# Kernel optimization log

Measured on AMD Instinct MI355X. Metric: run time of the kernel, lower is better.

## Reference

```python
import jax, jax.numpy as jnp
import numpy as np
import math

B, S, H, D = 4, 4096, 1024, 128

def setup_inputs() -> dict:
    key = jax.random.key(0)
    ks = jax.random.split(key, 4)
    scale = 1.0 / math.sqrt(H)
    return {
        "x": jax.random.normal(ks[0], (B, S, H), dtype=jnp.float32),
        "Wk": jax.random.normal(ks[1], (H, D), dtype=jnp.float32) * scale,
        "bk": jnp.zeros((D,), dtype=jnp.float32),
        "Wq": jax.random.normal(ks[2], (H, D), dtype=jnp.float32) * scale,
        "bq": jnp.zeros((D,), dtype=jnp.float32),
        "Wv": jax.random.normal(ks[3], (H, D), dtype=jnp.float32) * scale,
        "bv": jnp.zeros((D,), dtype=jnp.float32),
    }

def reference(x, Wk, bk, Wq, bq, Wv, bv):
    seq_len = x.shape[1]
    k = x @ Wk + bk                     # [B,S,D]
    q = x @ Wq + bq                     # [B,S,D]
    v = x @ Wv + bv                     # [B,S,D]
    scores = jnp.einsum('bqd,bkd->bqk', q, k) / jnp.sqrt(jnp.float32(q.shape[-1]))
    causal = jnp.tril(jnp.ones((seq_len, seq_len), dtype=bool))
    scores = jnp.where(causal, scores, -jnp.inf)
    attn = jax.nn.softmax(scores, axis=-1)  # dropout p=0.0 -> identity
    return jnp.einsum('bqk,bkd->bqd', attn, v)
```

## Files before the change

### kernel.cpp

```cpp
#include <hip/hip_runtime.h>
#include <hip/hip_bf16.h>

typedef __attribute__((ext_vector_type(8))) __bf16 bf16x8;
typedef __attribute__((ext_vector_type(4))) float f32x4;

#define QSCALE (0.08838834764831845f * 1.4426950408889634f)
#define SLOT_BYTES 33792

static __device__ __forceinline__ int pack2(float a, float b) {
    union { __bf16 h[2]; int u; } x;
    x.h[0] = (__bf16)a; x.h[1] = (__bf16)b;
    return x.u;
}

static __device__ __forceinline__ void softmax_strip(f32x4 (&s)[4], float& mr, float& lr,
                                                     f32x4 (&o)[8], int hi) {
    float mloc = s[0][0];
#pragma unroll
    for (int ct = 0; ct < 4; ++ct)
#pragma unroll
        for (int r = 0; r < 4; ++r) mloc = fmaxf(mloc, s[ct][r]);
    mloc = fmaxf(mloc, __shfl_xor(mloc, 16));
    mloc = fmaxf(mloc, __shfl_xor(mloc, 32));

    float alpha = 1.f;
    if (!__all(mloc <= mr + 8.f)) {
        const float mn = fmaxf(mr, mloc);
        alpha = exp2f(mr - mn);
        mr = mn;
        float ao[4];
#pragma unroll
        for (int r = 0; r < 4; ++r) ao[r] = __shfl(alpha, hi * 4 + r);
#pragma unroll
        for (int dt = 0; dt < 8; ++dt)
#pragma unroll
            for (int r = 0; r < 4; ++r) o[dt][r] *= ao[r];
    }
    float rs = 0.f;
#pragma unroll
    for (int ct = 0; ct < 4; ++ct)
#pragma unroll
        for (int r = 0; r < 4; ++r) {
            const float pv = exp2f(s[ct][r] - mr);
            s[ct][r] = pv;
            rs += pv;
        }
    rs += __shfl_xor(rs, 16);
    rs += __shfl_xor(rs, 32);
    lr = lr * alpha + rs;
}

static __device__ __forceinline__ void store_v_perm(__bf16* V_lds, int row, int u, bf16x8 val) {
    union { bf16x8 v; int2 d[2]; } x; x.v = val;
    const int ua  = 4 * (u >> 2) + 2 * (u & 1);
    const int off = ((u >> 1) & 1) * 8;
    const int sw  = row & 7;
    char* base = (char*)V_lds + row * 128;
    *reinterpret_cast<int2*>(base + ((ua ^ sw) << 4) + off)       = x.d[0];
    *reinterpret_cast<int2*>(base + (((ua + 1) ^ sw) << 4) + off) = x.d[1];
}

__global__ __launch_bounds__(256) void prep_w(const float* __restrict__ Wq,
                                              const float* __restrict__ Wk,
                                              const float* __restrict__ Wv,
                                              __bf16* __restrict__ Wt) {
    __shared__ float tile[32][33];
    const int bid = blockIdx.x;
    const int p   = bid >> 7;
    const int rem = bid & 127;
    const int kt  = rem >> 2;
    const int ct  = rem & 3;
    const float* W = (p == 0) ? Wq : ((p == 1) ? Wk : Wv);
    const int tr = threadIdx.x >> 5;
    const int tc = threadIdx.x & 31;
#pragma unroll
    for (int pass = 0; pass < 4; ++pass) {
        const int k = kt * 32 + pass * 8 + tr;
        tile[pass * 8 + tr][tc] = W[k * 128 + ct * 32 + tc];
    }
    __syncthreads();
#pragma unroll
    for (int pass = 0; pass < 4; ++pass) {
        const int c = ct * 32 + pass * 8 + tr;
        Wt[p * 131072 + c * 1024 + kt * 32 + tc] = (__bf16)tile[tc][pass * 8 + tr];
    }
}

__global__ __launch_bounds__(512, 4) void qkv_gemm(const float* __restrict__ x,
                                                   const __bf16* __restrict__ Wt,
                                                   const float* __restrict__ bq,
                                                   const float* __restrict__ bk,
                                                   const float* __restrict__ bv,
                                                   __bf16* __restrict__ qws,
                                                   __bf16* __restrict__ kws,
                                                   __bf16* __restrict__ vT) {
    __shared__ __align__(16) char smem[53248];
    __bf16* B_lds = (__bf16*)smem;
    __bf16* A_lds = (__bf16*)(smem + 49152);

    const int tid = threadIdx.x;
    const int w   = tid >> 6;
    const int l   = tid & 63;
    const int lo  = l & 15;
    const int hi  = l >> 4;
    const int r0  = blockIdx.x * 32;
    const int wr  = w >> 2;
    const int wc  = w & 3;

    const int arow = tid >> 4, aq = tid & 15;

    bf16x8 bst[6];
    float4 ast;

    auto STAGE_LOAD = [&](int ks) {
#pragma unroll
        for (int j = 0; j < 6; ++j) {
            const int n = w * 6 + j;
            const int c = n * 8 + (l >> 3);
            const int u = l & 7;
            bst[j] = *reinterpret_cast<const bf16x8*>(
                Wt + (size_t)c * 1024 + ks * 64 + u * 8);
        }
        ast = *reinterpret_cast<const float4*>(
            x + (size_t)(r0 + arow) * 1024 + ks * 64 + aq * 4);
    };
    auto STAGE_WRITE = [&]() {
#pragma unroll
        for (int j = 0; j < 6; ++j) {
            const int n = w * 6 + j;
            const int c = n * 8 + (l >> 3);
            const int u = l & 7;
            *reinterpret_cast<bf16x8*>(&B_lds[c * 64 + ((u ^ (c & 7)) << 3)]) = bst[j];
        }
        union { __bf16 h[4]; int2 d; } av;
        av.h[0] = (__bf16)ast.x; av.h[1] = (__bf16)ast.y;
        av.h[2] = (__bf16)ast.z; av.h[3] = (__bf16)ast.w;
        *reinterpret_cast<int2*>((char*)A_lds + arow * 128 +
            (((aq >> 1) ^ (arow & 7)) << 4) + ((aq & 1) << 3)) = av.d;
    };

    f32x4 acc[6];
#pragma unroll
    for (int tt = 0; tt < 6; ++tt) acc[tt] = (f32x4){0.f, 0.f, 0.f, 0.f};

    STAGE_LOAD(0);
    STAGE_WRITE();
    __syncthreads();

    const int lr = wr * 16 + lo;
    for (int ks = 0; ks < 16; ++ks) {
        if (ks < 15) STAGE_LOAD(ks + 1);

#pragma unroll
        for (int kc = 0; kc < 2; ++kc) {
            bf16x8 a = *reinterpret_cast<const bf16x8*>(
                &A_lds[lr * 64 + (((kc * 4 + hi) ^ (lr & 7)) << 3)]);
#pragma unroll
            for (int tt = 0; tt < 6; ++tt) {
                const int c = (wc * 6 + tt) * 16 + lo;
                bf16x8 b = *reinterpret_cast<const bf16x8*>(
                    &B_lds[c * 64 + (((kc * 4 + hi) ^ (c & 7)) << 3)]);
                acc[tt] = __builtin_amdgcn_mfma_f32_16x16x32_bf16(a, b, acc[tt], 0, 0, 0);
            }
        }
        __syncthreads();
        if (ks < 15) {
            STAGE_WRITE();
            __syncthreads();
        }
    }

    __bf16* ob = (__bf16*)smem;
#pragma unroll
    for (int tt = 0; tt < 6; ++tt) {
        const int t    = wc * 6 + tt;
        const int proj = t >> 3;
        const int col  = (t & 7) * 16 + lo;
        const float* bias = (proj == 0) ? bq : ((proj == 1) ? bk : bv);
        const float bb = bias[col];
        const float sc = (proj == 0) ? QSCALE : 1.f;
#pragma unroll
        for (int r = 0; r < 4; ++r) {
            const int row = wr * 16 + hi * 4 + r;
            ob[row * 392 + t * 16 + lo] = (__bf16)((acc[tt][r] + bb) * sc);
        }
    }
    __syncthreads();

    {
        const int row = tid >> 4;
        const int ch  = tid & 15;
        bf16x8 vq = *reinterpret_cast<const bf16x8*>(&ob[row * 392 + ch * 8]);
        bf16x8 vk = *reinterpret_cast<const bf16x8*>(&ob[row * 392 + 128 + ch * 8]);
        *reinterpret_cast<bf16x8*>(&qws[(size_t)(r0 + row) * 128 + ch * 8]) = vq;
        *reinterpret_cast<bf16x8*>(&kws[(size_t)(r0 + row) * 128 + ch * 8]) = vk;
    }
    {
        const int col = tid >> 2;
        const int rc  = tid & 3;
        bf16x8 vv;
#pragma unroll
        for (int j = 0; j < 8; ++j)
            vv[j] = ob[(rc * 8 + j) * 392 + 256 + col];
        const int b_ = r0 >> 12;
        const int s0 = r0 & 4095;
        *reinterpret_cast<bf16x8*>(
            &vT[(size_t)b_ * 524288 + (size_t)col * 4096 + s0 + rc * 8]) = vv;
    }
}

__global__ __launch_bounds__(512, 4) void attn(const __bf16* __restrict__ qws,
                                               const __bf16* __restrict__ kws,
                                               const __bf16* __restrict__ vT,
                                               char* __restrict__ part,
                                               float* __restrict__ out,
                                               int NSEG, int SEG, int direct) {
    __shared__ __align__(16) __bf16 K_lds[2][64 * 128];
    __shared__ __align__(16) __bf16 V_lds[2][128 * 64];

    const int tid = threadIdx.x;
    const int w   = tid >> 6;
    const int l   = tid & 63;
    const int lo  = l & 15;
    const int hi  = l >> 4;

    const int sidx = blockIdx.x / NSEG;
    const int seg  = blockIdx.x - sidx * NSEG;
    const int batch = sidx & 3;
    const int mblk  = 31 - (sidx >> 2);
    const int q0    = mblk * 128;
    const int extent = q0 + 128;

    const int kv_start = seg * SEG;
    if (kv_start >= extent) return;
    const int kv_end = min(kv_start + SEG, extent);
    const int t0 = kv_start >> 6;
    const int t1 = (kv_end + 63) >> 6;

    const int rw = q0 + w * 16;

    const int tKrow = tid >> 3;
    const int tKu   = (tid & 7) * 2;
    const int tVrow = tid >> 2;
    const int tVu   = (tid & 3) * 2;

    const __bf16* kb = kws + (size_t)batch * 524288;
    const __bf16* vb = vT  + (size_t)batch * 524288;

    const size_t qoff = (size_t)(batch * 4096 + rw + lo) * 128 + hi * 8;
    bf16x8 qf[4];
#pragma unroll
    for (int dc = 0; dc < 4; ++dc)
        qf[dc] = *reinterpret_cast<const bf16x8*>(qws + qoff + dc * 32);

    {
        const int kvb = t0 * 64;
        bf16x8 k0 = *reinterpret_cast<const bf16x8*>(kb + (size_t)(kvb + tKrow) * 128 + tKu * 8);
        bf16x8 k1 = *reinterpret_cast<const bf16x8*>(kb + (size_t)(kvb + tKrow) * 128 + tKu * 8 + 8);
        bf16x8 v0 = *reinterpret_cast<const bf16x8*>(vb + (size_t)tVrow * 4096 + kvb + tVu * 8);
        bf16x8 v1 = *reinterpret_cast<const bf16x8*>(vb + (size_t)tVrow * 4096 + kvb + tVu * 8 + 8);
        *reinterpret_cast<bf16x8*>(&K_lds[0][tKrow * 128 + ((tKu       ^ (tKrow & 7)) * 8)]) = k0;
        *reinterpret_cast<bf16x8*>(&K_lds[0][tKrow * 128 + (((tKu + 1) ^ (tKrow & 7)) * 8)]) = k1;
        store_v_perm(V_lds[0], tVrow, tVu,     v0);
        store_v_perm(V_lds[0], tVrow, tVu + 1, v1);
        __syncthreads();
    }

    f32x4 o[8];
#pragma unroll
    for (int dt = 0; dt < 8; ++dt) o[dt] = (f32x4){0.f, 0.f, 0.f, 0.f};
    float mr = -__builtin_inff();
    float lr = 0.f;

    int cur = 0;
    for (int t = t0; t < t1; ++t) {
        const int kvb = t * 64;
        const bool pfetch = (t + 1 < t1);

        bf16x8 kr0, kr1, vr0, vr1;
        if (pfetch) {
            const int kvn = kvb + 64;
            kr0 = *reinterpret_cast<const bf16x8*>(kb + (size_t)(kvn + tKrow) * 128 + tKu * 8);
            kr1 = *reinterpret_cast<const bf16x8*>(kb + (size_t)(kvn + tKrow) * 128 + tKu * 8 + 8);
            vr0 = *reinterpret_cast<const bf16x8*>(vb + (size_t)tVrow * 4096 + kvn + tVu * 8);
            vr1 = *reinterpret_cast<const bf16x8*>(vb + (size_t)tVrow * 4096 + kvn + tVu * 8 + 8);
        }

        if (kvb <= rw + 15) {
            f32x4 s[4];
#pragma unroll
            for (int ct = 0; ct < 4; ++ct) s[ct] = (f32x4){0.f, 0.f, 0.f, 0.f};
            const int sw = lo & 7;
            __builtin_amdgcn_s_setprio(1);
#pragma unroll
            for (int ct = 0; ct < 4; ++ct) {
                const int rbase = (ct * 16 + lo) * 128;
#pragma unroll
                for (int dc = 0; dc < 4; ++dc) {
                    bf16x8 kf = *reinterpret_cast<const bf16x8*>(
                        &K_lds[cur][rbase + (((dc * 4 + hi) ^ sw) << 3)]);
                    s[ct] = __builtin_amdgcn_mfma_f32_16x16x32_bf16(kf, qf[dc], s[ct], 0, 0, 0);
                }
            }
            __builtin_amdgcn_s_setprio(0);

            if (kvb + 63 > rw) {
#pragma unroll
                for (int ct = 0; ct < 4; ++ct)
#pragma unroll
                    for (int r = 0; r < 4; ++r)
                        if (kvb + ct * 16 + hi * 4 + r > rw + lo)
                            s[ct][r] = -__builtin_inff();
            }

            softmax_strip(s, mr, lr, o, hi);

            union { int u[4]; bf16x8 v; } pf0, pf1;
            pf0.u[0] = pack2(s[0][0], s[0][1]);
            pf0.u[1] = pack2(s[0][2], s[0][3]);
            pf0.u[2] = pack2(s[1][0], s[1][1]);
            pf0.u[3] = pack2(s[1][2], s[1][3]);
            pf1.u[0] = pack2(s[2][0], s[2][1]);
            pf1.u[1] = pack2(s[2][2], s[2][3]);
            pf1.u[2] = pack2(s[3][0], s[3][1]);
            pf1.u[3] = pack2(s[3][2], s[3][3]);

            __builtin_amdgcn_s_setprio(1);
#pragma unroll
            for (int dt = 0; dt < 8; ++dt) {
                const int vbase = (dt * 16 + lo) * 64;
                bf16x8 vf0 = *reinterpret_cast<const bf16x8*>(
                    &V_lds[cur][vbase + ((hi ^ sw) << 3)]);
                o[dt] = __builtin_amdgcn_mfma_f32_16x16x32_bf16(pf0.v, vf0, o[dt], 0, 0, 0);
                bf16x8 vf1 = *reinterpret_cast<const bf16x8*>(
                    &V_lds[cur][vbase + (((4 + hi) ^ sw) << 3)]);
                o[dt] = __builtin_amdgcn_mfma_f32_16x16x32_bf16(pf1.v, vf1, o[dt], 0, 0, 0);
            }
            __builtin_amdgcn_s_setprio(0);
        }

        if (pfetch) {
            const int nxt = cur ^ 1;
            *reinterpret_cast<bf16x8*>(&K_lds[nxt][tKrow * 128 + ((tKu       ^ (tKrow & 7)) * 8)]) = kr0;
            *reinterpret_cast<bf16x8*>(&K_lds[nxt][tKrow * 128 + (((tKu + 1) ^ (tKrow & 7)) * 8)]) = kr1;
            store_v_perm(V_lds[nxt], tVrow, tVu,     vr0);
            store_v_perm(V_lds[nxt], tVrow, tVu + 1, vr1);
            __syncthreads();
            cur = nxt;
        }
    }

    float lro[4], mro[4];
#pragma unroll
    for (int r = 0; r < 4; ++r) {
        lro[r] = __shfl(lr, hi * 4 + r);
        mro[r] = __shfl(mr, hi * 4 + r);
    }

    if (direct) {
#pragma unroll
        for (int dt = 0; dt < 8; ++dt)
#pragma unroll
            for (int r = 0; r < 4; ++r) {
                const size_t row = (size_t)(batch * 4096 + rw + hi * 4 + r);
                out[row * 128 + dt * 16 + lo] = o[dt][r] / lro[r];
            }
    } else {
        char* slot = part + ((size_t)(sidx * NSEG + seg)) * SLOT_BYTES;
        __bf16* so = (__bf16*)slot;
        float*  sf = (float*)(slot + 32768);
        const int rb = w * 16 + hi * 4;
#pragma unroll
        for (int dt = 0; dt < 8; ++dt)
#pragma unroll
            for (int r = 0; r < 4; ++r)
                so[(rb + r) * 128 + dt * 16 + lo] = (__bf16)o[dt][r];
        if (lo == 0) {
#pragma unroll
            for (int r = 0; r < 4; ++r) {
                sf[rb + r]       = mro[r];
                sf[128 + rb + r] = lro[r];
            }
        }
    }
}

__global__ __launch_bounds__(256) void combine(const char* __restrict__ part,
                                               float* __restrict__ out,
                                               int NSEG, int SEG) {
    const int sidx = blockIdx.x >> 3;
    const int rg   = blockIdx.x & 7;
    const int batch = sidx & 3;
    const int mblk  = 31 - (sidx >> 2);
    const int extent = mblk * 128 + 128;
    const int nseg  = min(NSEG, (extent + SEG - 1) / SEG);

    const int rl = rg * 16 + (threadIdx.x >> 4);
    const int c0 = (threadIdx.x & 15) * 8;
    const char* base = part + (size_t)sidx * NSEG * SLOT_BYTES;

    float mj[8];
    float M = -__builtin_inff();
#pragma unroll 8
    for (int j = 0; j < 8; ++j) {
        if (j < nseg) {
            mj[j] = ((const float*)(base + j * SLOT_BYTES + 32768))[rl];
            M = fmaxf(M, mj[j]);
        }
    }
    float wj[8];
    float L = 0.f;
#pragma unroll 8
    for (int j = 0; j < 8; ++j) {
        if (j < nseg) {
            wj[j] = exp2f(mj[j] - M);
            L += ((const float*)(base + j * SLOT_BYTES + 32768))[128 + rl] * wj[j];
        }
    }

    float a[8];
#pragma unroll
    for (int e = 0; e < 8; ++e) a[e] = 0.f;
#pragma unroll 8
    for (int j = 0; j < 8; ++j) {
        if (j < nseg) {
            const bf16x8 ov = *reinterpret_cast<const bf16x8*>(
                base + j * SLOT_BYTES + (size_t)(rl * 128 + c0) * 2);
            const float wgt = wj[j];
#pragma unroll
            for (int e = 0; e < 8; ++e) a[e] += (float)ov[e] * wgt;
        }
    }
    const float inv = 1.f / L;
    float* op = out + ((size_t)(batch * 4096 + mblk * 128 + rl)) * 128 + c0;
    float4* o4 = reinterpret_cast<float4*>(op);
    o4[0] = (float4){a[0]*inv, a[1]*inv, a[2]*inv, a[3]*inv};
    o4[1] = (float4){a[4]*inv, a[5]*inv, a[6]*inv, a[7]*inv};
}

extern "C" void kernel_launch(void* const* d_in, const int* in_sizes, int n_in,
                              void* d_out, int out_size, void* d_ws, size_t ws_size,
                              hipStream_t stream) {
    const float* x  = (const float*)d_in[0];
    const float* Wk = (const float*)d_in[1];
    const float* bk = (const float*)d_in[2];
    const float* Wq = (const float*)d_in[3];
    const float* bq = (const float*)d_in[4];
    const float* Wv = (const float*)d_in[5];
    const float* bv = (const float*)d_in[6];
    float* out = (float*)d_out;

    char* ws = (char*)d_ws;
    __bf16* Wt  = (__bf16*)ws;
    __bf16* qws = (__bf16*)(ws + 786432);
    __bf16* kws = (__bf16*)(ws + 786432 + 4194304);
    __bf16* vT  = (__bf16*)(ws + 786432 + 2 * 4194304);
    const size_t base = 786432 + 3 * 4194304;

    const size_t per_seg = 128ull * SLOT_BYTES;
    int NSEG = 1;
    for (int cand = 8; cand >= 2; cand >>= 1) {
        if (base + (size_t)cand * per_seg <= ws_size) { NSEG = cand; break; }
    }
    char* part = ws + base;

    prep_w<<<384, 256, 0, stream>>>(Wq, Wk, Wv, Wt);
    qkv_gemm<<<512, 512, 0, stream>>>(x, Wt, bq, bk, bv, qws, kws, vT);

    if (NSEG >= 2) {
        const int SEG = 4096 / NSEG;
        attn<<<128 * NSEG, 512, 0, stream>>>(qws, kws, vT, part, out, NSEG, SEG, 0);
        combine<<<1024, 256, 0, stream>>>(part, out, NSEG, SEG);
    } else {
        attn<<<128, 512, 0, stream>>>(qws, kws, vT, nullptr, out, 1, 4096, 1);
    }
}
```

Before: 100.0 us.

## Double query rows per attention block and stage K via direct global-to-LDS loads

Each block now processes 256 query rows instead of 128, with every wave handling two 16-row strips that share the K and V fragments read from LDS. This halves K/V traffic per query row. K tiles are staged with global_load_lds directly into LDS, bypassing registers. The split-KV partitioning goes up to 16 segments, and the combine kernel and slot layout are resized to match. In exchange, accumulator register pressure roughly doubles, which can reduce occupancy. The second strip's Q is reloaded from global memory on every tile, and with fewer query blocks the causal load balance is coarser.

New measurement: 324.9 us. +224.8%, slower.

```diff
diff --git a/kernel.cpp b/kernel.cpp
--- a/kernel.cpp
+++ b/kernel.cpp
@@ -5,7 +5,7 @@
 typedef __attribute__((ext_vector_type(4))) float f32x4;
 
 #define QSCALE (0.08838834764831845f * 1.4426950408889634f)
-#define SLOT_BYTES 33792
+#define SLOT_BYTES 67584
 
 static __device__ __forceinline__ int pack2(float a, float b) {
     union { __bf16 h[2]; int u; } x;
@@ -227,9 +227,9 @@
     const int sidx = blockIdx.x / NSEG;
     const int seg  = blockIdx.x - sidx * NSEG;
     const int batch = sidx & 3;
-    const int mblk  = 31 - (sidx >> 2);
-    const int q0    = mblk * 128;
-    const int extent = q0 + 128;
+    const int mblk  = 15 - (sidx >> 2);
+    const int q0    = mblk * 256;
+    const int extent = q0 + 256;
 
     const int kv_start = seg * SEG;
     if (kv_start >= extent) return;
@@ -237,59 +237,84 @@
     const int t0 = kv_start >> 6;
     const int t1 = (kv_end + 63) >> 6;
 
-    const int rw = q0 + w * 16;
-
-    const int tKrow = tid >> 3;
-    const int tKu   = (tid & 7) * 2;
+    const int rwA = q0 + w * 32;
+    const int rwB = rwA + 16;
+
     const int tVrow = tid >> 2;
     const int tVu   = (tid & 3) * 2;
 
     const __bf16* kb = kws + (size_t)batch * 524288;
     const __bf16* vb = vT  + (size_t)batch * 524288;
 
-    const size_t qoff = (size_t)(batch * 4096 + rw + lo) * 128 + hi * 8;
-    bf16x8 qf[4];
+    auto stage_k = [&](int buf, int kvb) {
+#pragma unroll
+        for (int j = 0; j < 2; ++j) {
+            const int c   = w * 2 + j;
+            const int row = c * 4 + (l >> 4);
+            const int up  = l & 15;
+            const __bf16* g = kb + (size_t)(kvb + row) * 128 + ((up ^ (row & 7)) << 3);
+            __builtin_amdgcn_global_load_lds(
+                (const __attribute__((address_space(1))) void*)g,
+                (__attribute__((address_space(3))) void*)&K_lds[buf][c * 512],
+                16, 0, 0);
+        }
+    };
+
+    const size_t qoffA = (size_t)(batch * 4096 + rwA + lo) * 128 + hi * 8;
+    const size_t qoffB = qoffA + 16 * 128;
+    bf16x8 qfA[4];
 #pragma unroll
     for (int dc = 0; dc < 4; ++dc)
-        qf[dc] = *reinterpret_cast<const bf16x8*>(qws + qoff + dc * 32);
+        qfA[dc] = *reinterpret_cast<const bf16x8*>(qws + qoffA + dc * 32);
 
     {
         const int kvb = t0 * 64;
-        bf16x8 k0 = *reinterpret_cast<const bf16x8*>(kb + (size_t)(kvb + tKrow) * 128 + tKu * 8);
-        bf16x8 k1 = *reinterpret_cast<const bf16x8*>(kb + (size_t)(kvb + tKrow) * 128 + tKu * 8 + 8);
+        stage_k(0, kvb);
         bf16x8 v0 = *reinterpret_cast<const bf16x8*>(vb + (size_t)tVrow * 4096 + kvb + tVu * 8);
         bf16x8 v1 = *reinterpret_cast<const bf16x8*>(vb + (size_t)tVrow * 4096 + kvb + tVu * 8 + 8);
-        *reinterpret_cast<bf16x8*>(&K_lds[0][tKrow * 128 + ((tKu       ^ (tKrow & 7)) * 8)]) = k0;
-        *reinterpret_cast<bf16x8*>(&K_lds[0][tKrow * 128 + (((tKu + 1) ^ (tKrow & 7)) * 8)]) = k1;
         store_v_perm(V_lds[0], tVrow, tVu,     v0);
         store_v_perm(V_lds[0], tVrow, tVu + 1, v1);
         __syncthreads();
     }
 
-    f32x4 o[8];
-#pragma unroll
-    for (int dt = 0; dt < 8; ++dt) o[dt] = (f32x4){0.f, 0.f, 0.f, 0.f};
-    float mr = -__builtin_inff();
-    float lr = 0.f;
+    f32x4 oA[8], oB[8];
+#pragma unroll
+    for (int dt = 0; dt < 8; ++dt) {
+        oA[dt] = (f32x4){0.f, 0.f, 0.f, 0.f};
+        oB[dt] = (f32x4){0.f, 0.f, 0.f, 0.f};
+    }
+    float mrA = -__builtin_inff(), lrA = 0.f;
+    float mrB = -__builtin_inff(), lrB = 0.f;
 
     int cur = 0;
     for (int t = t0; t < t1; ++t) {
         const int kvb = t * 64;
         const bool pfetch = (t + 1 < t1);
-
-        bf16x8 kr0, kr1, vr0, vr1;
+        const int nxt = cur ^ 1;
+
+        bf16x8 vr0, vr1;
         if (pfetch) {
             const int kvn = kvb + 64;
-            kr0 = *reinterpret_cast<const bf16x8*>(kb + (size_t)(kvn + tKrow) * 128 + tKu * 8);
-            kr1 = *reinterpret_cast<const bf16x8*>(kb + (size_t)(kvn + tKrow) * 128 + tKu * 8 + 8);
+            stage_k(nxt, kvn);
             vr0 = *reinterpret_cast<const bf16x8*>(vb + (size_t)tVrow * 4096 + kvn + tVu * 8);
             vr1 = *reinterpret_cast<const bf16x8*>(vb + (size_t)tVrow * 4096 + kvn + tVu * 8 + 8);
         }
 
-        if (kvb <= rw + 15) {
-            f32x4 s[4];
-#pragma unroll
-            for (int ct = 0; ct < 4; ++ct) s[ct] = (f32x4){0.f, 0.f, 0.f, 0.f};
+        const bool doB = (kvb <= rwB + 15);
+        const bool doA = (kvb <= rwA + 15);
+
+        if (doB) {
+            bf16x8 qfB[4];
+#pragma unroll
+            for (int dc = 0; dc < 4; ++dc)
+                qfB[dc] = *reinterpret_cast<const bf16x8*>(qws + qoffB + dc * 32);
+
+            f32x4 sA[4], sB[4];
+#pragma unroll
+            for (int ct = 0; ct < 4; ++ct) {
+                sA[ct] = (f32x4){0.f, 0.f, 0.f, 0.f};
+                sB[ct] = (f32x4){0.f, 0.f, 0.f, 0.f};
+            }
             const int sw = lo & 7;
             __builtin_amdgcn_s_setprio(1);
 #pragma unroll
@@ -299,31 +324,51 @@
                 for (int dc = 0; dc < 4; ++dc) {
                     bf16x8 kf = *reinterpret_cast<const bf16x8*>(
                         &K_lds[cur][rbase + (((dc * 4 + hi) ^ sw) << 3)]);
-                    s[ct] = __builtin_amdgcn_mfma_f32_16x16x32_bf16(kf, qf[dc], s[ct], 0, 0, 0);
+                    sB[ct] = __builtin_amdgcn_mfma_f32_16x16x32_bf16(kf, qfB[dc], sB[ct], 0, 0, 0);
+                    if (doA)
+                        sA[ct] = __builtin_amdgcn_mfma_f32_16x16x32_bf16(kf, qfA[dc], sA[ct], 0, 0, 0);
                 }
             }
             __builtin_amdgcn_s_setprio(0);
 
-            if (kvb + 63 > rw) {
+            if (kvb + 63 > rwB) {
 #pragma unroll
                 for (int ct = 0; ct < 4; ++ct)
 #pragma unroll
                     for (int r = 0; r < 4; ++r)
-                        if (kvb + ct * 16 + hi * 4 + r > rw + lo)
-                            s[ct][r] = -__builtin_inff();
-            }
-
-            softmax_strip(s, mr, lr, o, hi);
-
-            union { int u[4]; bf16x8 v; } pf0, pf1;
-            pf0.u[0] = pack2(s[0][0], s[0][1]);
-            pf0.u[1] = pack2(s[0][2], s[0][3]);
-            pf0.u[2] = pack2(s[1][0], s[1][1]);
-            pf0.u[3] = pack2(s[1][2], s[1][3]);
-            pf1.u[0] = pack2(s[2][0], s[2][1]);
-            pf1.u[1] = pack2(s[2][2], s[2][3]);
-            pf1.u[2] = pack2(s[3][0], s[3][1]);
-            pf1.u[3] = pack2(s[3][2], s[3][3]);
+                        if (kvb + ct * 16 + hi * 4 + r > rwB + lo)
+                            sB[ct][r] = -__builtin_inff();
+            }
+            if (doA && kvb + 63 > rwA) {
+#pragma unroll
+                for (int ct = 0; ct < 4; ++ct)
+#pragma unroll
+                    for (int r = 0; r < 4; ++r)
+                        if (kvb + ct * 16 + hi * 4 + r > rwA + lo)
+                            sA[ct][r] = -__builtin_inff();
+            }
+
+            softmax_strip(sB, mrB, lrB, oB, hi);
+            union { int u[4]; bf16x8 v; } pfB0, pfB1, pfA0, pfA1;
+            pfB0.u[0] = pack2(sB[0][0], sB[0][1]);
+            pfB0.u[1] = pack2(sB[0][2], sB[0][3]);
+            pfB0.u[2] = pack2(sB[1][0], sB[1][1]);
+            pfB0.u[3] = pack2(sB[1][2], sB[1][3]);
+            pfB1.u[0] = pack2(sB[2][0], sB[2][1]);
+            pfB1.u[1] = pack2(sB[2][2], sB[2][3]);
+            pfB1.u[2] = pack2(sB[3][0], sB[3][1]);
+            pfB1.u[3] = pack2(sB[3][2], sB[3][3]);
+            if (doA) {
+                softmax_strip(sA, mrA, lrA, oA, hi);
+                pfA0.u[0] = pack2(sA[0][0], sA[0][1]);
+                pfA0.u[1] = pack2(sA[0][2], sA[0][3]);
+                pfA0.u[2] = pack2(sA[1][0], sA[1][1]);
+                pfA0.u[3] = pack2(sA[1][2], sA[1][3]);
+                pfA1.u[0] = pack2(sA[2][0], sA[2][1]);
+                pfA1.u[1] = pack2(sA[2][2], sA[2][3]);
+                pfA1.u[2] = pack2(sA[3][0], sA[3][1]);
+                pfA1.u[3] = pack2(sA[3][2], sA[3][3]);
+            }
 
             __builtin_amdgcn_s_setprio(1);
 #pragma unroll
@@ -331,18 +376,19 @@
                 const int vbase = (dt * 16 + lo) * 64;
                 bf16x8 vf0 = *reinterpret_cast<const bf16x8*>(
                     &V_lds[cur][vbase + ((hi ^ sw) << 3)]);
-                o[dt] = __builtin_amdgcn_mfma_f32_16x16x32_bf16(pf0.v, vf0, o[dt], 0, 0, 0);
                 bf16x8 vf1 = *reinterpret_cast<const bf16x8*>(
                     &V_lds[cur][vbase + (((4 + hi) ^ sw) << 3)]);
-                o[dt] = __builtin_amdgcn_mfma_f32_16x16x32_bf16(pf1.v, vf1, o[dt], 0, 0, 0);
+                oB[dt] = __builtin_amdgcn_mfma_f32_16x16x32_bf16(pfB0.v, vf0, oB[dt], 0, 0, 0);
+                oB[dt] = __builtin_amdgcn_mfma_f32_16x16x32_bf16(pfB1.v, vf1, oB[dt], 0, 0, 0);
+                if (doA) {
+                    oA[dt] = __builtin_amdgcn_mfma_f32_16x16x32_bf16(pfA0.v, vf0, oA[dt], 0, 0, 0);
+                    oA[dt] = __builtin_amdgcn_mfma_f32_16x16x32_bf16(pfA1.v, vf1, oA[dt], 0, 0, 0);
+                }
             }
             __builtin_amdgcn_s_setprio(0);
         }
 
         if (pfetch) {
-            const int nxt = cur ^ 1;
-            *reinterpret_cast<bf16x8*>(&K_lds[nxt][tKrow * 128 + ((tKu       ^ (tKrow & 7)) * 8)]) = kr0;
-            *reinterpret_cast<bf16x8*>(&K_lds[nxt][tKrow * 128 + (((tKu + 1) ^ (tKrow & 7)) * 8)]) = kr1;
             store_v_perm(V_lds[nxt], tVrow, tVu,     vr0);
             store_v_perm(V_lds[nxt], tVrow, tVu + 1, vr1);
             __syncthreads();
@@ -350,11 +396,13 @@
         }
     }
 
-    float lro[4], mro[4];
+    float lroA[4], mroA[4], lroB[4], mroB[4];
 #pragma unroll
     for (int r = 0; r < 4; ++r) {
-        lro[r] = __shfl(lr, hi * 4 + r);
-        mro[r] = __shfl(mr, hi * 4 + r);
+        lroA[r] = __shfl(lrA, hi * 4 + r);
+        mroA[r] = __shfl(mrA, hi * 4 + r);
+        lroB[r] = __shfl(lrB, hi * 4 + r);
+        mroB[r] = __shfl(mrB, hi * 4 + r);
     }
 
     if (direct) {
@@ -362,24 +410,30 @@
         for (int dt = 0; dt < 8; ++dt)
 #pragma unroll
             for (int r = 0; r < 4; ++r) {
-                const size_t row = (size_t)(batch * 4096 + rw + hi * 4 + r);
-                out[row * 128 + dt * 16 + lo] = o[dt][r] / lro[r];
+                const size_t rowA = (size_t)(batch * 4096 + rwA + hi * 4 + r);
+                out[rowA * 128 + dt * 16 + lo] = oA[dt][r] / lroA[r];
+                out[(rowA + 16) * 128 + dt * 16 + lo] = oB[dt][r] / lroB[r];
             }
     } else {
         char* slot = part + ((size_t)(sidx * NSEG + seg)) * SLOT_BYTES;
         __bf16* so = (__bf16*)slot;
-        float*  sf = (float*)(slot + 32768);
-        const int rb = w * 16 + hi * 4;
+        float*  sm = (float*)(slot + 65536);
+        float*  sl = (float*)(slot + 66560);
+        const int rb = w * 32 + hi * 4;
 #pragma unroll
         for (int dt = 0; dt < 8; ++dt)
 #pragma unroll
-            for (int r = 0; r < 4; ++r)
-                so[(rb + r) * 128 + dt * 16 + lo] = (__bf16)o[dt][r];
+            for (int r = 0; r < 4; ++r) {
+                so[(rb + r) * 128 + dt * 16 + lo]      = (__bf16)oA[dt][r];
+                so[(rb + 16 + r) * 128 + dt * 16 + lo] = (__bf16)oB[dt][r];
+            }
         if (lo == 0) {
 #pragma unroll
             for (int r = 0; r < 4; ++r) {
-                sf[rb + r]       = mro[r];
-                sf[128 + rb + r] = lro[r];
+                sm[rb + r]      = mroA[r];
+                sl[rb + r]      = lroA[r];
+                sm[rb + 16 + r] = mroB[r];
+                sl[rb + 16 + r] = lroB[r];
             }
         }
     }
@@ -388,41 +442,41 @@
 __global__ __launch_bounds__(256) void combine(const char* __restrict__ part,
                                                float* __restrict__ out,
                                                int NSEG, int SEG) {
-    const int sidx = blockIdx.x >> 3;
-    const int rg   = blockIdx.x & 7;
+    const int sidx = blockIdx.x >> 4;
+    const int rg   = blockIdx.x & 15;
     const int batch = sidx & 3;
-    const int mblk  = 31 - (sidx >> 2);
-    const int extent = mblk * 128 + 128;
+    const int mblk  = 15 - (sidx >> 2);
+    const int extent = mblk * 256 + 256;
     const int nseg  = min(NSEG, (extent + SEG - 1) / SEG);
 
     const int rl = rg * 16 + (threadIdx.x >> 4);
     const int c0 = (threadIdx.x & 15) * 8;
     const char* base = part + (size_t)sidx * NSEG * SLOT_BYTES;
 
-    float mj[8];
+    float mj[16];
     float M = -__builtin_inff();
-#pragma unroll 8
-    for (int j = 0; j < 8; ++j) {
+#pragma unroll 16
+    for (int j = 0; j < 16; ++j) {
         if (j < nseg) {
-            mj[j] = ((const float*)(base + j * SLOT_BYTES + 32768))[rl];
+            mj[j] = ((const float*)(base + j * SLOT_BYTES + 65536))[rl];
             M = fmaxf(M, mj[j]);
         }
     }
-    float wj[8];
+    float wj[16];
     float L = 0.f;
-#pragma unroll 8
-    for (int j = 0; j < 8; ++j) {
+#pragma unroll 16
+    for (int j = 0; j < 16; ++j) {
         if (j < nseg) {
             wj[j] = exp2f(mj[j] - M);
-            L += ((const float*)(base + j * SLOT_BYTES + 32768))[128 + rl] * wj[j];
+            L += ((const float*)(base + j * SLOT_BYTES + 66560))[rl] * wj[j];
         }
     }
 
     float a[8];
 #pragma unroll
     for (int e = 0; e < 8; ++e) a[e] = 0.f;
-#pragma unroll 8
-    for (int j = 0; j < 8; ++j) {
+#pragma unroll 16
+    for (int j = 0; j < 16; ++j) {
         if (j < nseg) {
             const bf16x8 ov = *reinterpret_cast<const bf16x8*>(
                 base + j * SLOT_BYTES + (size_t)(rl * 128 + c0) * 2);
@@ -432,7 +486,7 @@
         }
     }
     const float inv = 1.f / L;
-    float* op = out + ((size_t)(batch * 4096 + mblk * 128 + rl)) * 128 + c0;
+    float* op = out + ((size_t)(batch * 4096 + mblk * 256 + rl)) * 128 + c0;
     float4* o4 = reinterpret_cast<float4*>(op);
     o4[0] = (float4){a[0]*inv, a[1]*inv, a[2]*inv, a[3]*inv};
     o4[1] = (float4){a[4]*inv, a[5]*inv, a[6]*inv, a[7]*inv};
@@ -457,9 +511,9 @@
     __bf16* vT  = (__bf16*)(ws + 786432 + 2 * 4194304);
     const size_t base = 786432 + 3 * 4194304;
 
-    const size_t per_seg = 128ull * SLOT_BYTES;
+    const size_t per_seg = 64ull * SLOT_BYTES;
     int NSEG = 1;
-    for (int cand = 8; cand >= 2; cand >>= 1) {
+    for (int cand = 16; cand >= 2; cand >>= 1) {
         if (base + (size_t)cand * per_seg <= ws_size) { NSEG = cand; break; }
     }
     char* part = ws + base;
@@ -469,9 +523,9 @@
 
     if (NSEG >= 2) {
         const int SEG = 4096 / NSEG;
-        attn<<<128 * NSEG, 512, 0, stream>>>(qws, kws, vT, part, out, NSEG, SEG, 0);
+        attn<<<64 * NSEG, 512, 0, stream>>>(qws, kws, vT, part, out, NSEG, SEG, 0);
         combine<<<1024, 256, 0, stream>>>(part, out, NSEG, SEG);
     } else {
-        attn<<<128, 512, 0, stream>>>(qws, kws, vT, nullptr, out, 1, 4096, 1);
-    }
-}
+        attn<<<64, 512, 0, stream>>>(qws, kws, vT, nullptr, out, 1, 4096, 1);
+    }
+}
```

## Software-pipeline QK of next tile with softmax/PV of current tile

Applied to the files above, without the earlier changes.

Restructures the attention inner loop so the QK^T MFMAs for tile t+1 are issued before the softmax and PV work for tile t, using ping-pong score registers unrolled by two. Global loads are prefetched two tiles ahead, and LDS commits are bracketed by two barriers. The aim is to overlap the softmax VALU work with matrix-core work and hide load latency. In exchange it uses more registers for the second score set and adds an extra barrier per iteration, which could lower occupancy.

Measured after the change: 116.9 us. +16.9%, slower.

```diff
diff --git a/kernel.cpp b/kernel.cpp
--- a/kernel.cpp
+++ b/kernel.cpp
@@ -238,6 +238,7 @@
     const int t1 = (kv_end + 63) >> 6;
 
     const int rw = q0 + w * 16;
+    const int sw = lo & 7;
 
     const int tKrow = tid >> 3;
     const int tKu   = (tid & 7) * 2;
@@ -253,102 +254,109 @@
     for (int dc = 0; dc < 4; ++dc)
         qf[dc] = *reinterpret_cast<const bf16x8*>(qws + qoff + dc * 32);
 
-    {
-        const int kvb = t0 * 64;
-        bf16x8 k0 = *reinterpret_cast<const bf16x8*>(kb + (size_t)(kvb + tKrow) * 128 + tKu * 8);
-        bf16x8 k1 = *reinterpret_cast<const bf16x8*>(kb + (size_t)(kvb + tKrow) * 128 + tKu * 8 + 8);
-        bf16x8 v0 = *reinterpret_cast<const bf16x8*>(vb + (size_t)tVrow * 4096 + kvb + tVu * 8);
-        bf16x8 v1 = *reinterpret_cast<const bf16x8*>(vb + (size_t)tVrow * 4096 + kvb + tVu * 8 + 8);
-        *reinterpret_cast<bf16x8*>(&K_lds[0][tKrow * 128 + ((tKu       ^ (tKrow & 7)) * 8)]) = k0;
-        *reinterpret_cast<bf16x8*>(&K_lds[0][tKrow * 128 + (((tKu + 1) ^ (tKrow & 7)) * 8)]) = k1;
-        store_v_perm(V_lds[0], tVrow, tVu,     v0);
-        store_v_perm(V_lds[0], tVrow, tVu + 1, v1);
-        __syncthreads();
-    }
-
     f32x4 o[8];
 #pragma unroll
     for (int dt = 0; dt < 8; ++dt) o[dt] = (f32x4){0.f, 0.f, 0.f, 0.f};
     float mr = -__builtin_inff();
     float lr = 0.f;
 
+    bf16x8 kr0, kr1, vr0, vr1;
+
+    auto LOADT = [&](int kvb) {
+        kr0 = *reinterpret_cast<const bf16x8*>(kb + (size_t)(kvb + tKrow) * 128 + tKu * 8);
+        kr1 = *reinterpret_cast<const bf16x8*>(kb + (size_t)(kvb + tKrow) * 128 + tKu * 8 + 8);
+        vr0 = *reinterpret_cast<const bf16x8*>(vb + (size_t)tVrow * 4096 + kvb + tVu * 8);
+        vr1 = *reinterpret_cast<const bf16x8*>(vb + (size_t)tVrow * 4096 + kvb + tVu * 8 + 8);
+    };
+    auto COMMIT = [&](int buf) {
+        *reinterpret_cast<bf16x8*>(&K_lds[buf][tKrow * 128 + ((tKu       ^ (tKrow & 7)) * 8)]) = kr0;
+        *reinterpret_cast<bf16x8*>(&K_lds[buf][tKrow * 128 + (((tKu + 1) ^ (tKrow & 7)) * 8)]) = kr1;
+        store_v_perm(V_lds[buf], tVrow, tVu,     vr0);
+        store_v_perm(V_lds[buf], tVrow, tVu + 1, vr1);
+    };
+    auto QK = [&](int buf, f32x4 (&s)[4]) {
+#pragma unroll
+        for (int ct = 0; ct < 4; ++ct) s[ct] = (f32x4){0.f, 0.f, 0.f, 0.f};
+        __builtin_amdgcn_s_setprio(1);
+#pragma unroll
+        for (int ct = 0; ct < 4; ++ct) {
+            const int rbase = (ct * 16 + lo) * 128;
+#pragma unroll
+            for (int dc = 0; dc < 4; ++dc) {
+                bf16x8 kf = *reinterpret_cast<const bf16x8*>(
+                    &K_lds[buf][rbase + (((dc * 4 + hi) ^ sw) << 3)]);
+                s[ct] = __builtin_amdgcn_mfma_f32_16x16x32_bf16(kf, qf[dc], s[ct], 0, 0, 0);
+            }
+        }
+        __builtin_amdgcn_s_setprio(0);
+    };
+    auto PROC = [&](int t, int buf, f32x4 (&s)[4]) {
+        const int kvb = t * 64;
+        if (kvb + 63 > rw) {
+#pragma unroll
+            for (int ct = 0; ct < 4; ++ct)
+#pragma unroll
+                for (int r = 0; r < 4; ++r)
+                    if (kvb + ct * 16 + hi * 4 + r > rw + lo)
+                        s[ct][r] = -__builtin_inff();
+        }
+        softmax_strip(s, mr, lr, o, hi);
+        union { int u[4]; bf16x8 v; } pf0, pf1;
+        pf0.u[0] = pack2(s[0][0], s[0][1]);
+        pf0.u[1] = pack2(s[0][2], s[0][3]);
+        pf0.u[2] = pack2(s[1][0], s[1][1]);
+        pf0.u[3] = pack2(s[1][2], s[1][3]);
+        pf1.u[0] = pack2(s[2][0], s[2][1]);
+        pf1.u[1] = pack2(s[2][2], s[2][3]);
+        pf1.u[2] = pack2(s[3][0], s[3][1]);
+        pf1.u[3] = pack2(s[3][2], s[3][3]);
+        __builtin_amdgcn_s_setprio(1);
+#pragma unroll
+        for (int dt = 0; dt < 8; ++dt) {
+            const int vbase = (dt * 16 + lo) * 64;
+            bf16x8 vf0 = *reinterpret_cast<const bf16x8*>(
+                &V_lds[buf][vbase + ((hi ^ sw) << 3)]);
+            o[dt] = __builtin_amdgcn_mfma_f32_16x16x32_bf16(pf0.v, vf0, o[dt], 0, 0, 0);
+            bf16x8 vf1 = *reinterpret_cast<const bf16x8*>(
+                &V_lds[buf][vbase + (((4 + hi) ^ sw) << 3)]);
+            o[dt] = __builtin_amdgcn_mfma_f32_16x16x32_bf16(pf1.v, vf1, o[dt], 0, 0, 0);
+        }
+        __builtin_amdgcn_s_setprio(0);
+    };
+
+    LOADT(t0 * 64);
+    COMMIT(0);
+    if (t0 + 1 < t1) LOADT((t0 + 1) * 64);
+    __syncthreads();
+
+    f32x4 sA[4], sB[4];
+    if (t0 * 64 <= rw + 15) QK(0, sA);
+
+#define PIPE_ITER(SIN, SOUT)                                                  \
+    {                                                                         \
+        const bool has_n1 = (t + 1 < t1);                                     \
+        if (has_n1) {                                                         \
+            const int nb = cur ^ 1;                                           \
+            __syncthreads();                   \
+            COMMIT(nb);                                                       \
+            __syncthreads();                            \
+            if (t + 2 < t1) LOADT((t + 2) * 64);                              \
+            if ((t + 1) * 64 <= rw + 15) QK(nb, SOUT);                        \
+        }                                                                     \
+        if (t * 64 <= rw + 15) PROC(t, cur, SIN);                             \
+        if (has_n1) cur ^= 1;                                                 \
+    }
+
     int cur = 0;
-    for (int t = t0; t < t1; ++t) {
-        const int kvb = t * 64;
-        const bool pfetch = (t + 1 < t1);
-
-        bf16x8 kr0, kr1, vr0, vr1;
-        if (pfetch) {
-            const int kvn = kvb + 64;
-            kr0 = *reinterpret_cast<const bf16x8*>(kb + (size_t)(kvn + tKrow) * 128 + tKu * 8);
-            kr1 = *reinterpret_cast<const bf16x8*>(kb + (size_t)(kvn + tKrow) * 128 + tKu * 8 + 8);
-            vr0 = *reinterpret_cast<const bf16x8*>(vb + (size_t)tVrow * 4096 + kvn + tVu * 8);
-            vr1 = *reinterpret_cast<const bf16x8*>(vb + (size_t)tVrow * 4096 + kvn + tVu * 8 + 8);
-        }
-
-        if (kvb <= rw + 15) {
-            f32x4 s[4];
-#pragma unroll
-            for (int ct = 0; ct < 4; ++ct) s[ct] = (f32x4){0.f, 0.f, 0.f, 0.f};
-            const int sw = lo & 7;
-            __builtin_amdgcn_s_setprio(1);
-#pragma unroll
-            for (int ct = 0; ct < 4; ++ct) {
-                const int rbase = (ct * 16 + lo) * 128;
-#pragma unroll
-                for (int dc = 0; dc < 4; ++dc) {
-                    bf16x8 kf = *reinterpret_cast<const bf16x8*>(
-                        &K_lds[cur][rbase + (((dc * 4 + hi) ^ sw) << 3)]);
-                    s[ct] = __builtin_amdgcn_mfma_f32_16x16x32_bf16(kf, qf[dc], s[ct], 0, 0, 0);
-                }
-            }
-            __builtin_amdgcn_s_setprio(0);
-
-            if (kvb + 63 > rw) {
-#pragma unroll
-                for (int ct = 0; ct < 4; ++ct)
-#pragma unroll
-                    for (int r = 0; r < 4; ++r)
-                        if (kvb + ct * 16 + hi * 4 + r > rw + lo)
-                            s[ct][r] = -__builtin_inff();
-            }
-
-            softmax_strip(s, mr, lr, o, hi);
-
-            union { int u[4]; bf16x8 v; } pf0, pf1;
-            pf0.u[0] = pack2(s[0][0], s[0][1]);
-            pf0.u[1] = pack2(s[0][2], s[0][3]);
-            pf0.u[2] = pack2(s[1][0], s[1][1]);
-            pf0.u[3] = pack2(s[1][2], s[1][3]);
-            pf1.u[0] = pack2(s[2][0], s[2][1]);
-            pf1.u[1] = pack2(s[2][2], s[2][3]);
-            pf1.u[2] = pack2(s[3][0], s[3][1]);
-            pf1.u[3] = pack2(s[3][2], s[3][3]);
-
-            __builtin_amdgcn_s_setprio(1);
-#pragma unroll
-            for (int dt = 0; dt < 8; ++dt) {
-                const int vbase = (dt * 16 + lo) * 64;
-                bf16x8 vf0 = *reinterpret_cast<const bf16x8*>(
-                    &V_lds[cur][vbase + ((hi ^ sw) << 3)]);
-                o[dt] = __builtin_amdgcn_mfma_f32_16x16x32_bf16(pf0.v, vf0, o[dt], 0, 0, 0);
-                bf16x8 vf1 = *reinterpret_cast<const bf16x8*>(
-                    &V_lds[cur][vbase + (((4 + hi) ^ sw) << 3)]);
-                o[dt] = __builtin_amdgcn_mfma_f32_16x16x32_bf16(pf1.v, vf1, o[dt], 0, 0, 0);
-            }
-            __builtin_amdgcn_s_setprio(0);
-        }
-
-        if (pfetch) {
-            const int nxt = cur ^ 1;
-            *reinterpret_cast<bf16x8*>(&K_lds[nxt][tKrow * 128 + ((tKu       ^ (tKrow & 7)) * 8)]) = kr0;
-            *reinterpret_cast<bf16x8*>(&K_lds[nxt][tKrow * 128 + (((tKu + 1) ^ (tKrow & 7)) * 8)]) = kr1;
-            store_v_perm(V_lds[nxt], tVrow, tVu,     vr0);
-            store_v_perm(V_lds[nxt], tVrow, tVu + 1, vr1);
-            __syncthreads();
-            cur = nxt;
-        }
-    }
+    int t = cur; t = t0;
+    while (t < t1) {
+        PIPE_ITER(sA, sB)
+        ++t;
+        if (t >= t1) break;
+        PIPE_ITER(sB, sA)
+        ++t;
+    }
+#undef PIPE_ITER
 
     float lro[4], mro[4];
 #pragma unroll
```
